# Optimization experiments

Hardware: AMD Instinct MI355X
Metric: run time of the kernel (lower is better)

## Reference

```python
import jax, jax.numpy as jnp
import numpy as np

# Bahdanau additive attention (eval mode: dropout is identity):
#   fac1 = W @ k        [B, d, S]
#   fac2 = U @ q        [B, d, S]
#   s    = v^T tanh(fac1 + fac2)   [B, 1, S]
#   attn = softmax(s, axis=-1)

B, D, S = 32, 1024, 2048


def setup_inputs() -> dict:
    key = jax.random.key(0)
    kq, kk, kv, kW, kU = jax.random.split(key, 5)
    scale = 1.0 / np.sqrt(D)
    return {
        "q": jax.random.normal(kq, (B, D, S), dtype=jnp.float32),
        "k": jax.random.normal(kk, (B, D, S), dtype=jnp.float32),
        "v": jax.random.normal(kv, (B, D, 1), dtype=jnp.float32),
        "W": jax.random.normal(kW, (D, D), dtype=jnp.float32) * scale,
        "U": jax.random.normal(kU, (D, D), dtype=jnp.float32) * scale,
    }


def reference(q, k, v, W, U):
    # projections: [d,e] x [b,e,s] -> [b,d,s]
    fac1 = jnp.einsum("de,bes->bds", W, k)
    fac2 = jnp.einsum("de,bes->bds", U, q)
    e = jnp.tanh(fac1 + fac2)            # [B, D, S]
    s = jnp.einsum("bdo,bds->bos", v, e)  # [B, 1, S]
    attn = jax.nn.softmax(s, axis=-1)     # softmax over sequence
    return attn
```

## Files before the change

kernel.cpp:

```cpp
#include <hip/hip_runtime.h>

#define D_ 1024
#define S_ 2048
#define B_ 32
#define BM 256
#define BN 256
#define BK 64
#define NKT 32

typedef __attribute__((ext_vector_type(8))) _Float16 f16x8;
typedef __attribute__((ext_vector_type(16))) float f32x16;

__device__ __forceinline__ void async_ld16(const void* g, void* l) {
  __builtin_amdgcn_global_load_lds(
      (const __attribute__((address_space(1))) void*)g,
      (__attribute__((address_space(3))) void*)l, 16, 0, 0);
}

__global__ void prep_kernel(const float* __restrict__ W, const float* __restrict__ U,
                            _Float16* __restrict__ wf, _Float16* __restrict__ uf) {
  int t = blockIdx.x * blockDim.x + threadIdx.x;
  const float* src = blockIdx.y ? U : W;
  _Float16* dst = blockIdx.y ? uf : wf;

  int tile = t >> 11;
  int g    = t & 2047;
  int top  = g >> 6;
  int ks = top >> 3, wr = (top >> 2) & 1, fm = top & 3;
  int lane = g & 63, l31 = lane & 31, lhi = lane >> 5;
  int row   = wr * 128 + fm * 32 + l31;
  int chunk = ks * 2 + lhi;
  int d = (tile >> 4) * 256 + row;
  int e = (tile & 15) * 64 + chunk * 8;

  const float* p = src + (size_t)d * D_ + e;
  f16x8 hv;
#pragma unroll
  for (int j = 0; j < 8; ++j) hv[j] = (_Float16)p[j];
  *(f16x8*)(dst + (size_t)t * 8) = hv;
}

__global__ void kqprep_kernel(const float* __restrict__ kten, const float* __restrict__ qten,
                              _Float16* __restrict__ bfmt) {
  size_t t = (size_t)blockIdx.x * 256 + threadIdx.x;
  int g    = (int)(t & 2047);
  int tile = (int)(t >> 11);
  int st   = tile & 7;
  int ktt  = (tile >> 3) & 15;
  int half = (tile >> 7) & 1;
  int b    = tile >> 8;
  int l31 = g & 31, clh = (g >> 5) & 1, w2 = (g >> 6) & 7, cks = g >> 9;
  int n = w2 * 32 + l31;
  int c = cks * 2 + clh;
  int e = ktt * 64 + c * 8;
  int s = st * 256 + n;

  const float* src = (half ? qten : kten) + (size_t)b * (D_ * S_) + (size_t)e * S_ + s;
  f16x8 hv;
#pragma unroll
  for (int j = 0; j < 8; ++j) hv[j] = (_Float16)src[(size_t)j * S_];
  *(f16x8*)(bfmt + t * 8) = hv;
}

__global__ void __launch_bounds__(512, 2)
gemm_kernel(const float* __restrict__ v,
            const _Float16* __restrict__ wf, const _Float16* __restrict__ uf,
            const _Float16* __restrict__ bfmt,
            float* __restrict__ partials) {
  __shared__ __align__(16) _Float16 Af[2][BM * BK];
  __shared__ __align__(16) _Float16 Bf[2][BN * BK];
  __shared__ float vbuf[BM];
  __shared__ float red[2][BN];

  const int tid  = threadIdx.x;
  const int lane = tid & 63;
  const int wid  = tid >> 6;
  const int wr   = wid >> 2;
  const int wc   = wid & 3;

  int bid  = blockIdx.x;
  int g    = ((bid >> 5) << 3) | (bid & 7);
  int dblk = (bid >> 3) & 3;
  int st   = g & 7;
  int b    = g >> 3;
  int s0   = st * BN;

  if (tid < BM) vbuf[tid] = v[(size_t)b * D_ + dblk * BM + tid];

  f32x16 acc[4][2];
#pragma unroll
  for (int i = 0; i < 4; ++i)
#pragma unroll
    for (int j = 0; j < 2; ++j)
#pragma unroll
      for (int r = 0; r < 16; ++r) acc[i][j][r] = 0.0f;

#define PH_FENCE asm volatile("" ::: "memory")

#define GLLA2(ktn, buf, part) do {                                             \
    const int half_ = (ktn) >> 4, ktt_ = (ktn) & 15;                           \
    const _Float16* at_ = (half_ ? uf : wf) + (size_t)(dblk * 16 + ktt_) * 16384; \
    async_ld16(at_ + (size_t)(tid + (part) * 1024) * 8,                        \
               &Af[buf][(size_t)(tid + (part) * 1024) * 8]);                   \
    async_ld16(at_ + (size_t)(tid + (part) * 1024 + 512) * 8,                  \
               &Af[buf][(size_t)(tid + (part) * 1024 + 512) * 8]);             \
  } while (0)

#define GLLB2(ktn, buf, part) do {                                             \
    const int half_ = (ktn) >> 4, ktt_ = (ktn) & 15;                           \
    const _Float16* bt_ = bfmt + ((size_t)(((b * 2 + half_) * 16 + ktt_) * 8 + st)) * 16384; \
    async_ld16(bt_ + (size_t)(tid + (part) * 1024) * 8,                        \
               &Bf[buf][(size_t)(tid + (part) * 1024) * 8]);                   \
    async_ld16(bt_ + (size_t)(tid + (part) * 1024 + 512) * 8,                  \
               &Bf[buf][(size_t)(tid + (part) * 1024 + 512) * 8]);             \
  } while (0)

#define WAIT4 asm volatile("s_waitcnt vmcnt(4)" ::: "memory")
#define WAIT0 asm volatile("s_waitcnt vmcnt(0)" ::: "memory")

#define PHASE(cur_, ks_, ISSUE, WAITC) do {                                    \
    PH_FENCE;                                                                  \
    f16x8 af_[4], bf_[2];                                                      \
    _Pragma("unroll")                                                          \
    for (int fm = 0; fm < 4; ++fm)                                             \
      af_[fm] = *(const f16x8*)&Af[cur_][(size_t)(((ks_) * 8 + wr * 4 + fm) * 64 + lane) * 8]; \
    _Pragma("unroll")                                                          \
    for (int fn = 0; fn < 2; ++fn)                                             \
      bf_[fn] = *(const f16x8*)&Bf[cur_][(size_t)(((ks_) * 8 + wc * 2 + fn) * 64 + lane) * 8]; \
    ISSUE;                                                                     \
    __builtin_amdgcn_s_barrier();                                              \
    __builtin_amdgcn_s_setprio(1);                                             \
    _Pragma("unroll")                                                          \
    for (int fm = 0; fm < 4; ++fm)                                             \
      _Pragma("unroll")                                                        \
      for (int fn = 0; fn < 2; ++fn)                                           \
        acc[fm][fn] = __builtin_amdgcn_mfma_f32_32x32x16_f16(af_[fm], bf_[fn], acc[fm][fn], 0, 0, 0); \
    __builtin_amdgcn_s_setprio(0);                                             \
    WAITC;                                                                     \
    __builtin_amdgcn_s_barrier();                                              \
    __builtin_amdgcn_sched_barrier(0);                                         \
  } while (0)

  PH_FENCE;
  GLLA2(0, 0, 0); GLLB2(0, 0, 0);
  GLLA2(0, 0, 1); GLLB2(0, 0, 1);
  WAIT4;
  __builtin_amdgcn_s_barrier();
  __builtin_amdgcn_sched_barrier(0);

  for (int kt = 0; kt < NKT - 1; ++kt) {
    const int cur = kt & 1, nxt = cur ^ 1;
    PHASE(cur, 0, GLLA2(kt + 1, nxt, 0), );
    PHASE(cur, 1, GLLB2(kt + 1, nxt, 0), WAIT4);
    PHASE(cur, 2, GLLA2(kt + 1, nxt, 1), );
    PHASE(cur, 3, GLLB2(kt + 1, nxt, 1), WAIT4);
  }
  PHASE(1, 0, , );
  PHASE(1, 1, , WAIT0);
  PHASE(1, 2, , );
  PHASE(1, 3, , );

#undef PHASE
#undef WAIT0
#undef WAIT4
#undef GLLB2
#undef GLLA2
#undef PH_FENCE

  float psum[2] = {0.f, 0.f};
#pragma unroll
  for (int fm = 0; fm < 4; ++fm)
#pragma unroll
    for (int fn = 0; fn < 2; ++fn)
#pragma unroll
      for (int r = 0; r < 16; ++r) {
        int row = wr * 128 + fm * 32 + (r & 3) + 8 * (r >> 2) + 4 * (lane >> 5);
        float x  = acc[fm][fn][r];
        float th = 1.0f - 2.0f / (__expf(2.0f * x) + 1.0f);
        psum[fn] += vbuf[row] * th;
      }
#pragma unroll
  for (int fn = 0; fn < 2; ++fn) psum[fn] += __shfl_xor(psum[fn], 32);
  if (lane < 32) {
    red[wr][wc * 64 + lane]      = psum[0];
    red[wr][wc * 64 + 32 + lane] = psum[1];
  }
  __syncthreads();
  if (tid < BN) {
    float val = red[0][tid] + red[1][tid];
    partials[(size_t)(dblk * B_ + b) * S_ + s0 + tid] = val;
  }
}

__global__ void __launch_bounds__(512, 2)
gemm_fb_kernel(const float* __restrict__ kten, const float* __restrict__ qten,
               const float* __restrict__ v,
               const _Float16* __restrict__ wf, const _Float16* __restrict__ uf,
               float* __restrict__ partials) {
  __shared__ __align__(16) _Float16 Af[2][BM * BK];
  __shared__ __align__(16) _Float16 Bf[2][BN * BK];
  __shared__ float vbuf[BM];
  __shared__ float red[2][BN];

  const int tid  = threadIdx.x;
  const int lane = tid & 63;
  const int wid  = tid >> 6;
  const int wr   = wid >> 2;
  const int wc   = wid & 3;

  int bid  = blockIdx.x;
  int g    = ((bid >> 5) << 3) | (bid & 7);
  int dblk = (bid >> 3) & 3;
  int st   = g & 7;
  int b    = g >> 3;
  int s0   = st * BN;

  if (tid < BM) vbuf[tid] = v[(size_t)b * D_ + dblk * BM + tid];

  f32x16 acc[4][2];
#pragma unroll
  for (int i = 0; i < 4; ++i)
#pragma unroll
    for (int j = 0; j < 2; ++j)
#pragma unroll
      for (int r = 0; r < 16; ++r) acc[i][j][r] = 0.0f;

  const int nB = tid & 255;
  const int kq = tid >> 8;

#define PH_FENCE_F asm volatile("" ::: "memory")
#define PH_BAR_F __builtin_amdgcn_s_barrier()

#define GLLA_F(ktn, buf, part) do {                                            \
    const int half_ = (ktn) >> 4, ktt_ = (ktn) & 15;                           \
    const _Float16* at_ = (half_ ? uf : wf) + (size_t)(dblk * 16 + ktt_) * 16384; \
    async_ld16(at_ + (size_t)(tid + (part) * 1024) * 8,                        \
               &Af[buf][(size_t)(tid + (part) * 1024) * 8]);                   \
    async_ld16(at_ + (size_t)(tid + (part) * 1024 + 512) * 8,                  \
               &Af[buf][(size_t)(tid + (part) * 1024 + 512) * 8]);             \
  } while (0)

#define LOADB_F(ktn, xv, h) do {                                               \
    const int half_ = (ktn) >> 4, ktt_ = (ktn) & 15;                           \
    const float* col_ = (half_ ? qten : kten) + (size_t)b * (D_ * S_)          \
                        + (size_t)(ktt_ * 64) * S_ + s0 + nB                   \
                        + (size_t)(kq * 32) * S_;                              \
    _Pragma("unroll")                                                          \
    for (int j = 16 * (h); j < 16 * (h) + 16; ++j) xv[j] = col_[(size_t)j * S_]; \
  } while (0)

#define CVTWRITE_F(xv, buf) do {                                               \
    _Pragma("unroll")                                                          \
    for (int cl = 0; cl < 4; ++cl) {                                           \
      f16x8 hv_;                                                               \
      _Pragma("unroll")                                                        \
      for (int w = 0; w < 8; ++w) hv_[w] = (_Float16)xv[cl * 8 + w];           \
      int c_ = kq * 4 + cl, cks_ = c_ >> 1, clh_ = c_ & 1;                     \
      int gnl_ = ((cks_ * 8 + (nB >> 6) * 2 + ((nB >> 5) & 1)) << 6)           \
                 | (clh_ << 5) | (nB & 31);                                    \
      *(f16x8*)&Bf[buf][(size_t)gnl_ * 8] = hv_;                               \
    }                                                                          \
  } while (0)

#define COMPUTE_PHASE_F(cur_, ks_) do {                                        \
    f16x8 af_[4], bf_[2];                                                      \
    _Pragma("unroll")                                                          \
    for (int fm = 0; fm < 4; ++fm)                                             \
      af_[fm] = *(const f16x8*)&Af[cur_][(size_t)(((ks_) * 8 + wr * 4 + fm) * 64 + lane) * 8]; \
    _Pragma("unroll")                                                          \
    for (int fn = 0; fn < 2; ++fn)                                             \
      bf_[fn] = *(const f16x8*)&Bf[cur_][(size_t)(((ks_) * 8 + wc * 2 + fn) * 64 + lane) * 8]; \
    __builtin_amdgcn_s_setprio(1);                                             \
    _Pragma("unroll")                                                          \
    for (int fm = 0; fm < 4; ++fm)                                             \
      _Pragma("unroll")                                                        \
      for (int fn = 0; fn < 2; ++fn)                                           \
        acc[fm][fn] = __builtin_amdgcn_mfma_f32_32x32x16_f16(af_[fm], bf_[fn], acc[fm][fn], 0, 0, 0); \
    __builtin_amdgcn_s_setprio(0);                                             \
  } while (0)

#define STEP_F(kt_, cur_, xvC_, xvN_) do {                                     \
    const int nxt_ = (cur_) ^ 1;                                               \
    PH_FENCE_F; GLLA_F((kt_) + 1, nxt_, 0); COMPUTE_PHASE_F(cur_, 0); PH_BAR_F;\
    PH_FENCE_F; GLLA_F((kt_) + 1, nxt_, 1); COMPUTE_PHASE_F(cur_, 1); PH_BAR_F;\
    PH_FENCE_F; LOADB_F((kt_) + 2, xvN_, 0); COMPUTE_PHASE_F(cur_, 2); PH_BAR_F;\
    PH_FENCE_F; LOADB_F((kt_) + 2, xvN_, 1); CVTWRITE_F(xvC_, nxt_);           \
              COMPUTE_PHASE_F(cur_, 3);                                        \
    asm volatile("s_waitcnt vmcnt(32) lgkmcnt(0)" ::: "memory");               \
    PH_BAR_F;                                                                  \
    __builtin_amdgcn_sched_barrier(0);                                         \
  } while (0)

  float xvA[32], xvB[32];
  LOADB_F(0, xvA, 0); LOADB_F(0, xvA, 1);
  GLLA_F(0, 0, 0);    GLLA_F(0, 0, 1);
  LOADB_F(1, xvB, 0); LOADB_F(1, xvB, 1);
  CVTWRITE_F(xvA, 0);
  __syncthreads();

  for (int it = 0; it < 15; ++it) {
    STEP_F(2 * it,     0, xvB, xvA);
    STEP_F(2 * it + 1, 1, xvA, xvB);
  }

  PH_FENCE_F; GLLA_F(31, 1, 0); COMPUTE_PHASE_F(0, 0); PH_BAR_F;
  PH_FENCE_F; GLLA_F(31, 1, 1); COMPUTE_PHASE_F(0, 1); PH_BAR_F;
  PH_FENCE_F; COMPUTE_PHASE_F(0, 2); PH_BAR_F;
  PH_FENCE_F; CVTWRITE_F(xvB, 1); COMPUTE_PHASE_F(0, 3);
  __syncthreads();
  COMPUTE_PHASE_F(1, 0); COMPUTE_PHASE_F(1, 1); COMPUTE_PHASE_F(1, 2); COMPUTE_PHASE_F(1, 3);

#undef STEP_F
#undef COMPUTE_PHASE_F
#undef CVTWRITE_F
#undef LOADB_F
#undef GLLA_F
#undef PH_BAR_F
#undef PH_FENCE_F

  float psum[2] = {0.f, 0.f};
#pragma unroll
  for (int fm = 0; fm < 4; ++fm)
#pragma unroll
    for (int fn = 0; fn < 2; ++fn)
#pragma unroll
      for (int r = 0; r < 16; ++r) {
        int row = wr * 128 + fm * 32 + (r & 3) + 8 * (r >> 2) + 4 * (lane >> 5);
        float x  = acc[fm][fn][r];
        float th = 1.0f - 2.0f / (__expf(2.0f * x) + 1.0f);
        psum[fn] += vbuf[row] * th;
      }
#pragma unroll
  for (int fn = 0; fn < 2; ++fn) psum[fn] += __shfl_xor(psum[fn], 32);
  if (lane < 32) {
    red[wr][wc * 64 + lane]      = psum[0];
    red[wr][wc * 64 + 32 + lane] = psum[1];
  }
  __syncthreads();
  if (tid < BN) {
    float val = red[0][tid] + red[1][tid];
    partials[(size_t)(dblk * B_ + b) * S_ + s0 + tid] = val;
  }
}

__global__ void softmax_kernel(const float* __restrict__ partials, float* __restrict__ out) {
  __shared__ float logit[S_];
  __shared__ float wred[2][4];
  int b = blockIdx.x, tid = threadIdx.x;
  int lane = tid & 63, wid = tid >> 6;
  float lmax = -1e30f;
  for (int i = tid; i < S_; i += 256) {
    float acc = 0.f;
#pragma unroll
    for (int d = 0; d < 4; ++d) acc += partials[(size_t)(d * B_ + b) * S_ + i];
    logit[i] = acc;
    lmax = fmaxf(lmax, acc);
  }
#pragma unroll
  for (int o = 32; o; o >>= 1) lmax = fmaxf(lmax, __shfl_xor(lmax, o));
  if (lane == 0) wred[0][wid] = lmax;
  __syncthreads();
  float m = fmaxf(fmaxf(wred[0][0], wred[0][1]), fmaxf(wred[0][2], wred[0][3]));
  float lsum = 0.f;
  for (int i = tid; i < S_; i += 256) {
    float ex = __expf(logit[i] - m);
    logit[i] = ex;
    lsum += ex;
  }
#pragma unroll
  for (int o = 32; o; o >>= 1) lsum += __shfl_xor(lsum, o);
  if (lane == 0) wred[1][wid] = lsum;
  __syncthreads();
  float tot = wred[1][0] + wred[1][1] + wred[1][2] + wred[1][3];
  float inv = 1.0f / tot;
  for (int i = tid; i < S_; i += 256) out[(size_t)b * S_ + i] = logit[i] * inv;
}

extern "C" void kernel_launch(void* const* d_in, const int* in_sizes, int n_in,
                              void* d_out, int out_size, void* d_ws, size_t ws_size,
                              hipStream_t stream) {
  const float* q = (const float*)d_in[0];
  const float* k = (const float*)d_in[1];
  const float* v = (const float*)d_in[2];
  const float* W = (const float*)d_in[3];
  const float* U = (const float*)d_in[4];

  _Float16* wf = (_Float16*)d_ws;
  _Float16* uf = wf + (size_t)D_ * D_;
  float* partials = (float*)(uf + (size_t)D_ * D_);
  _Float16* bfmt = (_Float16*)((char*)d_ws + 5242880);
  const size_t NEED = 5242880ull + 268435456ull;

  prep_kernel<<<dim3(512, 2), 256, 0, stream>>>(W, U, wf, uf);
  if (ws_size >= NEED) {
    kqprep_kernel<<<dim3(65536), 256, 0, stream>>>(k, q, bfmt);
    gemm_kernel<<<dim3(1024), 512, 0, stream>>>(v, wf, uf, bfmt, partials);
  } else {
    gemm_fb_kernel<<<dim3(1024), 512, 0, stream>>>(k, q, v, wf, uf, partials);
  }
  softmax_kernel<<<dim3(B_), 256, 0, stream>>>(partials, (float*)d_out);
}
```

Before: 461.9 us.

## Deepen GEMM pipeline to four half-tile LDS buffers with three loads in flight

Replaces the double-buffered full-K-tile scheme, which split each tile's loads across four phases, with four 32-wide-K half-tile buffers. Loads now run three phases ahead, and each phase issues A and B together and does two MFMA k-steps. The aim is to hide global-to-LDS latency better and halve the number of barrier phases. LDS use stays the same (4x half tiles), but each phase holds more fragment registers, which may add pressure at 2 waves per SIMD.

```diff
diff --git a/kernel.cpp b/kernel.cpp
--- a/kernel.cpp
+++ b/kernel.cpp
@@ -7,6 +7,7 @@
 #define BN 256
 #define BK 64
 #define NKT 32
+#define NPH 64
 
 typedef __attribute__((ext_vector_type(8))) _Float16 f16x8;
 typedef __attribute__((ext_vector_type(16))) float f32x16;
@@ -67,8 +68,8 @@
             const _Float16* __restrict__ wf, const _Float16* __restrict__ uf,
             const _Float16* __restrict__ bfmt,
             float* __restrict__ partials) {
-  __shared__ __align__(16) _Float16 Af[2][BM * BK];
-  __shared__ __align__(16) _Float16 Bf[2][BN * BK];
+  __shared__ __align__(16) _Float16 Af[4][BM * 32];
+  __shared__ __align__(16) _Float16 Bf[4][BN * 32];
   __shared__ float vbuf[BM];
   __shared__ float red[2][BN];
 
@@ -86,6 +87,7 @@
   int s0   = st * BN;
 
   if (tid < BM) vbuf[tid] = v[(size_t)b * D_ + dblk * BM + tid];
+  __syncthreads();
 
   f32x16 acc[4][2];
 #pragma unroll
@@ -96,37 +98,40 @@
       for (int r = 0; r < 16; ++r) acc[i][j][r] = 0.0f;
 
 #define PH_FENCE asm volatile("" ::: "memory")
-
-#define GLLA2(ktn, buf, part) do {                                             \
-    const int half_ = (ktn) >> 4, ktt_ = (ktn) & 15;                           \
-    const _Float16* at_ = (half_ ? uf : wf) + (size_t)(dblk * 16 + ktt_) * 16384; \
-    async_ld16(at_ + (size_t)(tid + (part) * 1024) * 8,                        \
-               &Af[buf][(size_t)(tid + (part) * 1024) * 8]);                   \
-    async_ld16(at_ + (size_t)(tid + (part) * 1024 + 512) * 8,                  \
-               &Af[buf][(size_t)(tid + (part) * 1024 + 512) * 8]);             \
-  } while (0)
-
-#define GLLB2(ktn, buf, part) do {                                             \
-    const int half_ = (ktn) >> 4, ktt_ = (ktn) & 15;                           \
-    const _Float16* bt_ = bfmt + ((size_t)(((b * 2 + half_) * 16 + ktt_) * 8 + st)) * 16384; \
-    async_ld16(bt_ + (size_t)(tid + (part) * 1024) * 8,                        \
-               &Bf[buf][(size_t)(tid + (part) * 1024) * 8]);                   \
-    async_ld16(bt_ + (size_t)(tid + (part) * 1024 + 512) * 8,                  \
-               &Bf[buf][(size_t)(tid + (part) * 1024 + 512) * 8]);             \
-  } while (0)
-
+#define WAIT8 asm volatile("s_waitcnt vmcnt(8)" ::: "memory")
 #define WAIT4 asm volatile("s_waitcnt vmcnt(4)" ::: "memory")
 #define WAIT0 asm volatile("s_waitcnt vmcnt(0)" ::: "memory")
 
-#define PHASE(cur_, ks_, ISSUE, WAITC) do {                                    \
+#define GLLH(h_) do {                                                          \
+    const int kt_ = (h_) >> 1, hh_ = (h_) & 1, bi_ = (h_) & 3;                 \
+    const int half_ = kt_ >> 4, ktt_ = kt_ & 15;                               \
+    const _Float16* at_ = (half_ ? uf : wf)                                    \
+        + (size_t)(dblk * 16 + ktt_) * 16384 + (size_t)hh_ * 8192;             \
+    const _Float16* bt_ = bfmt                                                 \
+        + ((size_t)(((b * 2 + half_) * 16 + ktt_) * 8 + st)) * 16384           \
+        + (size_t)hh_ * 8192;                                                  \
+    async_ld16(at_ + (size_t)tid * 8,         &Af[bi_][(size_t)tid * 8]);      \
+    async_ld16(at_ + (size_t)(tid + 512) * 8, &Af[bi_][(size_t)(tid + 512) * 8]); \
+    async_ld16(bt_ + (size_t)tid * 8,         &Bf[bi_][(size_t)tid * 8]);      \
+    async_ld16(bt_ + (size_t)(tid + 512) * 8, &Bf[bi_][(size_t)(tid + 512) * 8]); \
+  } while (0)
+
+#define PHASE(h_, ISSUE, WAITC) do {                                           \
     PH_FENCE;                                                                  \
-    f16x8 af_[4], bf_[2];                                                      \
-    _Pragma("unroll")                                                          \
-    for (int fm = 0; fm < 4; ++fm)                                             \
-      af_[fm] = *(const f16x8*)&Af[cur_][(size_t)(((ks_) * 8 + wr * 4 + fm) * 64 + lane) * 8]; \
+    const int bi_ = (h_) & 3;                                                  \
+    f16x8 a0_[4], a1_[4], b0_[2], b1_[2];                                      \
+    _Pragma("unroll")                                                          \
+    for (int fm = 0; fm < 4; ++fm)                                             \
+      a0_[fm] = *(const f16x8*)&Af[bi_][(size_t)(((wr * 4 + fm) * 64 + lane)) * 8]; \
     _Pragma("unroll")                                                          \
     for (int fn = 0; fn < 2; ++fn)                                             \
-      bf_[fn] = *(const f16x8*)&Bf[cur_][(size_t)(((ks_) * 8 + wc * 2 + fn) * 64 + lane) * 8]; \
+      b0_[fn] = *(const f16x8*)&Bf[bi_][(size_t)(((wc * 2 + fn) * 64 + lane)) * 8]; \
+    _Pragma("unroll")                                                          \
+    for (int fm = 0; fm < 4; ++fm)                                             \
+      a1_[fm] = *(const f16x8*)&Af[bi_][(size_t)(((8 + wr * 4 + fm) * 64 + lane)) * 8]; \
+    _Pragma("unroll")                                                          \
+    for (int fn = 0; fn < 2; ++fn)                                             \
+      b1_[fn] = *(const f16x8*)&Bf[bi_][(size_t)(((8 + wc * 2 + fn) * 64 + lane)) * 8]; \
     ISSUE;                                                                     \
     __builtin_amdgcn_s_barrier();                                              \
     __builtin_amdgcn_s_setprio(1);                                             \
@@ -134,7 +139,12 @@
     for (int fm = 0; fm < 4; ++fm)                                             \
       _Pragma("unroll")                                                        \
       for (int fn = 0; fn < 2; ++fn)                                           \
-        acc[fm][fn] = __builtin_amdgcn_mfma_f32_32x32x16_f16(af_[fm], bf_[fn], acc[fm][fn], 0, 0, 0); \
+        acc[fm][fn] = __builtin_amdgcn_mfma_f32_32x32x16_f16(a0_[fm], b0_[fn], acc[fm][fn], 0, 0, 0); \
+    _Pragma("unroll")                                                          \
+    for (int fm = 0; fm < 4; ++fm)                                             \
+      _Pragma("unroll")                                                        \
+      for (int fn = 0; fn < 2; ++fn)                                           \
+        acc[fm][fn] = __builtin_amdgcn_mfma_f32_32x32x16_f16(a1_[fm], b1_[fn], acc[fm][fn], 0, 0, 0); \
     __builtin_amdgcn_s_setprio(0);                                             \
     WAITC;                                                                     \
     __builtin_amdgcn_s_barrier();                                              \
@@ -142,29 +152,23 @@
   } while (0)
 
   PH_FENCE;
-  GLLA2(0, 0, 0); GLLB2(0, 0, 0);
-  GLLA2(0, 0, 1); GLLB2(0, 0, 1);
-  WAIT4;
+  GLLH(0); GLLH(1); GLLH(2);
+  WAIT8;
   __builtin_amdgcn_s_barrier();
   __builtin_amdgcn_sched_barrier(0);
 
-  for (int kt = 0; kt < NKT - 1; ++kt) {
-    const int cur = kt & 1, nxt = cur ^ 1;
-    PHASE(cur, 0, GLLA2(kt + 1, nxt, 0), );
-    PHASE(cur, 1, GLLB2(kt + 1, nxt, 0), WAIT4);
-    PHASE(cur, 2, GLLA2(kt + 1, nxt, 1), );
-    PHASE(cur, 3, GLLB2(kt + 1, nxt, 1), WAIT4);
-  }
-  PHASE(1, 0, , );
-  PHASE(1, 1, , WAIT0);
-  PHASE(1, 2, , );
-  PHASE(1, 3, , );
+  for (int h = 0; h < NPH - 3; ++h) {
+    PHASE(h, GLLH(h + 3), WAIT8);
+  }
+  PHASE(61, , WAIT4);
+  PHASE(62, , WAIT0);
+  PHASE(63, , );
 
 #undef PHASE
+#undef GLLH
 #undef WAIT0
 #undef WAIT4
-#undef GLLB2
-#undef GLLA2
+#undef WAIT8
 #undef PH_FENCE
 
   float psum[2] = {0.f, 0.f};
@@ -396,7 +400,7 @@
     kqprep_kernel<<<dim3(65536), 256, 0, stream>>>(k, q, bfmt);
     gemm_kernel<<<dim3(1024), 512, 0, stream>>>(v, wf, uf, bfmt, partials);
   } else {
-    gemm_fb_kernel<<<dim3(1024), 512, 0, stream>>>(k, q, v, wf, uf, partials);
+    gemm_fb_kernel<<<dim3(2048 / 2), 512, 0, stream>>>(k, q, v, wf, uf, partials);
   }
   softmax_kernel<<<dim3(B_), 256, 0, stream>>>(partials, (float*)d_out);
 }
```

New measurement: 418.0 us. 9.5% less time.
